# Performance work log

Measured on AMD Instinct MI355X. Metric: run time of the kernel, lower is better.

Reference implementation:

```python
import jax, jax.numpy as jnp
import numpy as np

N_SUBJECTS = 16
N_LABELS = 8
DENS_TEMP = 0.1  # args.ProtoSim_dens_temp


def setup_inputs() -> dict:
    key = jax.random.key(0)
    k1, k2, k3 = jax.random.split(key, 3)
    B, V, D = 131072, 2, 128
    X_data = jax.random.normal(k1, (B, V, D), dtype=jnp.float32)
    subject = jax.random.randint(k2, (B,), 0, N_SUBJECTS, dtype=jnp.int64) if jax.config.read('jax_enable_x64') else jax.random.randint(k2, (B,), 0, N_SUBJECTS)
    labels = jax.random.randint(k3, (B,), 0, N_LABELS)
    return {"X_data": X_data, "subject": subject, "labels": labels}


def reference(X_data, subject, labels):
    B, V, D = X_data.shape
    G = N_SUBJECTS * N_LABELS
    # torch.cat(torch.unbind(X_data, dim=1), dim=0): view-major ordering -> [V*B, D]
    cf = jnp.transpose(X_data, (1, 0, 2)).reshape(V * B, D)
    # subject/labels duplicated once (module assumes 2 views)
    seg = jnp.tile(subject * N_LABELS + labels, V)  # group id per row, [V*B]
    counts = jax.ops.segment_sum(jnp.ones((V * B,), jnp.float32), seg, num_segments=G)
    centroid = jax.ops.segment_sum(cf, seg, num_segments=G) / counts[:, None]  # [G, D]
    # per-point euclidean distance to own group centroid (torch.cdist to 1-row centroid)
    dist = jnp.linalg.norm(cf - centroid[seg], axis=1)  # [V*B]
    # density: mean(sqrt(dist)) / log(n + 10) for groups with n > 1, else 0 then dmax
    dens = (jax.ops.segment_sum(jnp.sqrt(dist), seg, num_segments=G) / counts) / jnp.log(counts + 10.0)
    dens = jnp.where(counts > 1, dens, 0.0)
    dens = jnp.where(counts > 1, dens, dens.max())
    lo = jnp.percentile(dens, 10.0)
    hi = jnp.percentile(dens, 90.0)
    dens = jnp.clip(dens, lo, hi)
    dens = DENS_TEMP * dens / dens.mean()
    cen_of_cen = centroid.mean(axis=0)  # [D]
    sim = jnp.exp((centroid @ cen_of_cen) / dens)  # [G]
    sim = sim - sim.max()
    return -sim.mean()
```

## Files before the change

kernel.cpp:

```cpp
#include <hip/hip_runtime.h>
#include <cstdint>
#include <cstddef>

#define BPTS    131072
#define D_DIM   128
#define G_GR    128
#define NL      8
#define NSLC    16
#define PERMBUF 128
#define NBLK_S  64
#define PPB     (BPTS / NBLK_S)

__global__ __launch_bounds__(256) void k_hist(const int* __restrict__ sub,
                                              const int* __restrict__ lab,
                                              int* __restrict__ hblk) {
    __shared__ int h[G_GR];
    int t = threadIdx.x, blk = blockIdx.x;
    if (t < G_GR) h[t] = 0;
    __syncthreads();
    int b0 = blk * PPB;
    for (int i = t; i < PPB; i += 256)
        atomicAdd(&h[sub[b0 + i] * NL + lab[b0 + i]], 1);
    __syncthreads();
    if (t < G_GR) hblk[blk * G_GR + t] = h[t];
}

__global__ __launch_bounds__(256) void k_scatter(const int* __restrict__ sub,
                                                 const int* __restrict__ lab,
                                                 const int* __restrict__ hblk,
                                                 int* __restrict__ counts,
                                                 int* __restrict__ offsets,
                                                 float* __restrict__ countsf,
                                                 int* __restrict__ perm) {
    __shared__ int tot[G_GR];
    __shared__ int cur[G_GR];
    int t = threadIdx.x, blk = blockIdx.x;
    if (t < G_GR) {
        int tt = 0, mine = 0;
        for (int b = 0; b < NBLK_S; ++b) {
            int v = hblk[b * G_GR + t];
            tt += v;
            if (b < blk) mine += v;
        }
        tot[t] = tt;
        cur[t] = mine;
    }
    __syncthreads();
    if (t < G_GR) {
        int off = 0;
        for (int j = 0; j < t; ++j) off += tot[j];
        cur[t] += off;
        if (blk == 0) {
            counts[t]  = tot[t];
            offsets[t] = off;
            countsf[t] = 2.0f * (float)tot[t];
        }
    }
    __syncthreads();
    int b0 = blk * PPB;
    for (int i = t; i < PPB; i += 256) {
        int p = b0 + i;
        int g = sub[p] * NL + lab[p];
        int s = atomicAdd(&cur[g], 1);
        perm[s] = p;
    }
}

__global__ __launch_bounds__(256) void k_psum(const float4* __restrict__ X4,
                                              const int* __restrict__ perm,
                                              const int* __restrict__ offsets,
                                              const int* __restrict__ counts,
                                              float* __restrict__ part) {
    __shared__ int   pbuf[PERMBUF];
    __shared__ float red[4 * 256];
    int g = blockIdx.x >> 4, s = blockIdx.x & 15;
    int off = offsets[g], len = counts[g];
    int lo = off + (len * s) / NSLC;
    int hi = off + (len * (s + 1)) / NSLC;
    int slen = hi - lo;
    int t = threadIdx.x, lane = t & 63, w = t >> 6;

    for (int j = t; j < slen; j += 256) pbuf[j] = perm[lo + j];
    __syncthreads();

    float4 acc = make_float4(0.f, 0.f, 0.f, 0.f);
    for (int i = w * 8; i < slen; i += 32) {
        int idx[8];
#pragma unroll
        for (int u = 0; u < 8; ++u) {
            int j = i + u;
            idx[u] = pbuf[(j < slen) ? j : (slen - 1)];
        }
        float4 x[8];
#pragma unroll
        for (int u = 0; u < 8; ++u) x[u] = X4[(size_t)idx[u] * 64 + lane];
#pragma unroll
        for (int u = 0; u < 8; ++u) {
            if (i + u < slen) {
                acc.x += x[u].x; acc.y += x[u].y;
                acc.z += x[u].z; acc.w += x[u].w;
            }
        }
    }
    red[w * 256 + lane * 4 + 0] = acc.x;
    red[w * 256 + lane * 4 + 1] = acc.y;
    red[w * 256 + lane * 4 + 2] = acc.z;
    red[w * 256 + lane * 4 + 3] = acc.w;
    __syncthreads();
    if (t < 128) {
        float v = 0.f;
        for (int r = 0; r < 4; ++r)
            v += red[r * 256 + t] + red[r * 256 + t + 128];
        part[(size_t)blockIdx.x * 128 + t] = v;
    }
}

__global__ __launch_bounds__(256) void k_dist(const float4* __restrict__ X4,
                                              const int* __restrict__ perm,
                                              const int* __restrict__ offsets,
                                              const int* __restrict__ counts,
                                              const float* __restrict__ part,
                                              float* __restrict__ centroid,
                                              float* __restrict__ dpart) {
    __shared__ int   pbuf[PERMBUF];
    __shared__ float cen[D_DIM];
    __shared__ float wsum[4];
    int g = blockIdx.x >> 4, s = blockIdx.x & 15;
    int off = offsets[g], len = counts[g];
    int lo = off + (len * s) / NSLC;
    int hi = off + (len * (s + 1)) / NSLC;
    int slen = hi - lo;
    int t = threadIdx.x, lane = t & 63, w = t >> 6;

    if (t < D_DIM) {
        float v = 0.f;
        for (int s2 = 0; s2 < NSLC; ++s2)
            v += part[(size_t)(g * NSLC + s2) * 128 + t];
        float c = (len > 0) ? v / (2.0f * (float)len) : 0.f;
        cen[t] = c;
        if (s == 0) centroid[g * D_DIM + t] = c;
    }
    for (int j = t; j < slen; j += 256) pbuf[j] = perm[lo + j];
    __syncthreads();

    int cd = (lane & 31) * 4;
    float4 c = make_float4(cen[cd], cen[cd + 1], cen[cd + 2], cen[cd + 3]);

    float sacc = 0.f;
    for (int i = w * 8; i < slen; i += 32) {
        int idx[8];
#pragma unroll
        for (int u = 0; u < 8; ++u) {
            int j = i + u;
            idx[u] = pbuf[(j < slen) ? j : (slen - 1)];
        }
        float4 x[8];
#pragma unroll
        for (int u = 0; u < 8; ++u) x[u] = X4[(size_t)idx[u] * 64 + lane];
#pragma unroll
        for (int u = 0; u < 8; ++u) {
            float dx = x[u].x - c.x, dy = x[u].y - c.y;
            float dz = x[u].z - c.z, dw = x[u].w - c.w;
            float d = dx * dx + dy * dy + dz * dz + dw * dw;
#pragma unroll
            for (int m = 1; m <= 16; m <<= 1) d += __shfl_xor(d, m);
            if (i + u < slen) sacc += sqrtf(sqrtf(d));
        }
    }
    float t2 = sacc + __shfl_xor(sacc, 32);
    if (lane == 0) wsum[w] = t2;
    __syncthreads();
    if (t == 0) dpart[blockIdx.x] = wsum[0] + wsum[1] + wsum[2] + wsum[3];
}

__global__ __launch_bounds__(128) void k_final(const float* __restrict__ dpart,
                                               const float* __restrict__ countsf,
                                               const float* __restrict__ centroid,
                                               float* __restrict__ out) {
    __shared__ float srt[G_GR];
    __shared__ float red[G_GR];
    __shared__ float coc[D_DIM];
    int t = threadIdx.x;

    float ds = 0.f;
    for (int s = 0; s < NSLC; ++s) ds += dpart[t * NSLC + s];
    float cnt  = countsf[t];
    float dens = (cnt > 1.f) ? (ds / cnt) / logf(cnt + 10.f) : 0.f;

    red[t] = dens;
    __syncthreads();
    for (int s = 64; s > 0; s >>= 1) {
        if (t < s) red[t] = fmaxf(red[t], red[t + s]);
        __syncthreads();
    }
    float dmax = red[0];
    __syncthreads();
    if (!(cnt > 1.f)) dens = dmax;

    srt[t] = dens;
    __syncthreads();
    for (int k = 2; k <= G_GR; k <<= 1) {
        for (int j = k >> 1; j > 0; j >>= 1) {
            int ixj = t ^ j;
            if (ixj > t) {
                float a = srt[t], b = srt[ixj];
                bool up = ((t & k) == 0);
                if ((a > b) == up) { srt[t] = b; srt[ixj] = a; }
            }
            __syncthreads();
        }
    }
    double p10 = 0.10 * 127.0, p90 = 0.90 * 127.0;
    int   i10 = (int)p10,           i90 = (int)p90;
    float f10 = (float)(p10 - i10), f90 = (float)(p90 - i90);
    float lo = srt[i10] + f10 * (srt[i10 + 1] - srt[i10]);
    float hi = srt[i90] + f90 * (srt[i90 + 1] - srt[i90]);
    dens = fminf(fmaxf(dens, lo), hi);

    red[t] = dens;
    __syncthreads();
    for (int s = 64; s > 0; s >>= 1) {
        if (t < s) red[t] += red[t + s];
        __syncthreads();
    }
    float dmean = red[0] / 128.f;
    __syncthreads();
    dens = 0.1f * dens / dmean;

    float cs = 0.f;
    for (int g = 0; g < G_GR; ++g) cs += centroid[g * D_DIM + t];
    coc[t] = cs / 128.f;
    __syncthreads();

    float dot = 0.f;
    for (int d = 0; d < D_DIM; ++d) dot += centroid[t * D_DIM + d] * coc[d];
    float sim = expf(dot / dens);

    red[t] = sim;
    __syncthreads();
    for (int s = 64; s > 0; s >>= 1) {
        if (t < s) red[t] = fmaxf(red[t], red[t + s]);
        __syncthreads();
    }
    float smax = red[0];
    __syncthreads();
    red[t] = sim - smax;
    __syncthreads();
    for (int s = 64; s > 0; s >>= 1) {
        if (t < s) red[t] += red[t + s];
        __syncthreads();
    }
    if (t == 0) out[0] = -(red[0] / 128.f);
}

extern "C" void kernel_launch(void* const* d_in, const int* in_sizes, int n_in,
                              void* d_out, int out_size, void* d_ws, size_t ws_size,
                              hipStream_t stream) {
    const float4* X4      = (const float4*)d_in[0];
    const int*    subject = (const int*)d_in[1];
    const int*    labels  = (const int*)d_in[2];
    float*        out     = (float*)d_out;
    char*         ws      = (char*)d_ws;

    size_t o = 0;
    int*   hblk     = (int*)(ws + o);   o += (size_t)NBLK_S * G_GR * 4;
    int*   counts   = (int*)(ws + o);   o += 512;
    int*   offsets  = (int*)(ws + o);   o += 512;
    float* countsf  = (float*)(ws + o); o += 512;
    int*   perm     = (int*)(ws + o);   o += (size_t)BPTS * 4;
    float* part     = (float*)(ws + o); o += (size_t)G_GR * NSLC * 128 * 4;
    float* centroid = (float*)(ws + o); o += (size_t)G_GR * D_DIM * 4;
    float* dpart    = (float*)(ws + o); o += (size_t)G_GR * NSLC * 4;

    k_hist   <<<NBLK_S, 256, 0, stream>>>(subject, labels, hblk);
    k_scatter<<<NBLK_S, 256, 0, stream>>>(subject, labels, hblk, counts, offsets, countsf, perm);
    k_psum   <<<G_GR * NSLC, 256, 0, stream>>>(X4, perm, offsets, counts, part);
    k_dist   <<<G_GR * NSLC, 256, 0, stream>>>(X4, perm, offsets, counts, part, centroid, dpart);
    k_final  <<<1, 128, 0, stream>>>(dpart, countsf, centroid, out);
}
```

Measured before the change: 240.2 us.

## Replace group sort with streaming LDS-atomic centroid and distance binning

Removes the histogram/scatter permutation and gathered per-group reads. Instead, each block streams contiguous points and accumulates per-group sums and distances into shared-memory bins with atomics. Per-block partials are then reduced by separate kernels. The trade is coalesced X reads against large partial-buffer traffic (512 copies of the 128x128 centroid bins), heavy LDS atomics, and 64KB LDS per block limiting occupancy.

Measured after the change: 300.8 us. +25.2%, slower.

```diff
diff --git a/kernel.cpp b/kernel.cpp
--- a/kernel.cpp
+++ b/kernel.cpp
@@ -6,174 +6,158 @@
 #define D_DIM   128
 #define G_GR    128
 #define NL      8
-#define NSLC    16
-#define PERMBUF 128
-#define NBLK_S  64
-#define PPB     (BPTS / NBLK_S)
-
-__global__ __launch_bounds__(256) void k_hist(const int* __restrict__ sub,
-                                              const int* __restrict__ lab,
-                                              int* __restrict__ hblk) {
-    __shared__ int h[G_GR];
+#define GD      (G_GR * D_DIM)
+#define NBLK    512
+#define TPB     512
+#define PPB     (BPTS / NBLK)
+#define PPW     (PPB / 8)
+#define DRB     16
+
+__global__ __launch_bounds__(TPB) void k_centroid(const float4* __restrict__ X4,
+                                                  const int* __restrict__ sub,
+                                                  const int* __restrict__ lab,
+                                                  float* __restrict__ cpart,
+                                                  int* __restrict__ hpart) {
+    __shared__ float bins[GD];
+    __shared__ int   hist[G_GR];
     int t = threadIdx.x, blk = blockIdx.x;
-    if (t < G_GR) h[t] = 0;
-    __syncthreads();
-    int b0 = blk * PPB;
-    for (int i = t; i < PPB; i += 256)
-        atomicAdd(&h[sub[b0 + i] * NL + lab[b0 + i]], 1);
-    __syncthreads();
-    if (t < G_GR) hblk[blk * G_GR + t] = h[t];
-}
-
-__global__ __launch_bounds__(256) void k_scatter(const int* __restrict__ sub,
-                                                 const int* __restrict__ lab,
-                                                 const int* __restrict__ hblk,
-                                                 int* __restrict__ counts,
-                                                 int* __restrict__ offsets,
-                                                 float* __restrict__ countsf,
-                                                 int* __restrict__ perm) {
-    __shared__ int tot[G_GR];
-    __shared__ int cur[G_GR];
-    int t = threadIdx.x, blk = blockIdx.x;
-    if (t < G_GR) {
-        int tt = 0, mine = 0;
-        for (int b = 0; b < NBLK_S; ++b) {
-            int v = hblk[b * G_GR + t];
-            tt += v;
-            if (b < blk) mine += v;
-        }
-        tot[t] = tt;
-        cur[t] = mine;
-    }
-    __syncthreads();
-    if (t < G_GR) {
-        int off = 0;
-        for (int j = 0; j < t; ++j) off += tot[j];
-        cur[t] += off;
-        if (blk == 0) {
-            counts[t]  = tot[t];
-            offsets[t] = off;
-            countsf[t] = 2.0f * (float)tot[t];
-        }
-    }
-    __syncthreads();
-    int b0 = blk * PPB;
-    for (int i = t; i < PPB; i += 256) {
-        int p = b0 + i;
-        int g = sub[p] * NL + lab[p];
-        int s = atomicAdd(&cur[g], 1);
-        perm[s] = p;
-    }
-}
-
-__global__ __launch_bounds__(256) void k_psum(const float4* __restrict__ X4,
-                                              const int* __restrict__ perm,
-                                              const int* __restrict__ offsets,
-                                              const int* __restrict__ counts,
-                                              float* __restrict__ part) {
-    __shared__ int   pbuf[PERMBUF];
-    __shared__ float red[4 * 256];
-    int g = blockIdx.x >> 4, s = blockIdx.x & 15;
-    int off = offsets[g], len = counts[g];
-    int lo = off + (len * s) / NSLC;
-    int hi = off + (len * (s + 1)) / NSLC;
-    int slen = hi - lo;
-    int t = threadIdx.x, lane = t & 63, w = t >> 6;
-
-    for (int j = t; j < slen; j += 256) pbuf[j] = perm[lo + j];
-    __syncthreads();
-
-    float4 acc = make_float4(0.f, 0.f, 0.f, 0.f);
-    for (int i = w * 8; i < slen; i += 32) {
-        int idx[8];
+    int lane = t & 63, w = t >> 6;
+
+    for (int i = t; i < GD; i += TPB) bins[i] = 0.f;
+    if (t < G_GR) hist[t] = 0;
+
+    int base = blk * PPB + w * PPW;
+    int pl = base + (lane & 31);
+    int gv = sub[pl] * NL + lab[pl];
+    __syncthreads();
+
+    for (int it = 0; it < PPW / 8; ++it) {
+        int p0 = base + it * 8;
+        float4 x[8];
+#pragma unroll
+        for (int u = 0; u < 8; ++u)
+            x[u] = X4[(size_t)(p0 + u) * 64 + lane];
 #pragma unroll
         for (int u = 0; u < 8; ++u) {
-            int j = i + u;
-            idx[u] = pbuf[(j < slen) ? j : (slen - 1)];
-        }
-        float4 x[8];
-#pragma unroll
-        for (int u = 0; u < 8; ++u) x[u] = X4[(size_t)idx[u] * 64 + lane];
-#pragma unroll
-        for (int u = 0; u < 8; ++u) {
-            if (i + u < slen) {
-                acc.x += x[u].x; acc.y += x[u].y;
-                acc.z += x[u].z; acc.w += x[u].w;
+            int g = __shfl(gv, it * 8 + u);
+            float4 v = x[u];
+            v.x += __shfl_xor(v.x, 32);
+            v.y += __shfl_xor(v.y, 32);
+            v.z += __shfl_xor(v.z, 32);
+            v.w += __shfl_xor(v.w, 32);
+            if (lane < 32) {
+                float* b = &bins[g * D_DIM + lane * 4];
+                atomicAdd(b + 0, v.x);
+                atomicAdd(b + 1, v.y);
+                atomicAdd(b + 2, v.z);
+                atomicAdd(b + 3, v.w);
+            } else if (lane == 32) {
+                atomicAdd(&hist[g], 1);
             }
         }
     }
-    red[w * 256 + lane * 4 + 0] = acc.x;
-    red[w * 256 + lane * 4 + 1] = acc.y;
-    red[w * 256 + lane * 4 + 2] = acc.z;
-    red[w * 256 + lane * 4 + 3] = acc.w;
-    __syncthreads();
-    if (t < 128) {
-        float v = 0.f;
-        for (int r = 0; r < 4; ++r)
-            v += red[r * 256 + t] + red[r * 256 + t + 128];
-        part[(size_t)blockIdx.x * 128 + t] = v;
-    }
-}
-
-__global__ __launch_bounds__(256) void k_dist(const float4* __restrict__ X4,
-                                              const int* __restrict__ perm,
-                                              const int* __restrict__ offsets,
-                                              const int* __restrict__ counts,
-                                              const float* __restrict__ part,
-                                              float* __restrict__ centroid,
-                                              float* __restrict__ dpart) {
-    __shared__ int   pbuf[PERMBUF];
-    __shared__ float cen[D_DIM];
-    __shared__ float wsum[4];
-    int g = blockIdx.x >> 4, s = blockIdx.x & 15;
-    int off = offsets[g], len = counts[g];
-    int lo = off + (len * s) / NSLC;
-    int hi = off + (len * (s + 1)) / NSLC;
-    int slen = hi - lo;
-    int t = threadIdx.x, lane = t & 63, w = t >> 6;
-
+    __syncthreads();
+    for (int i = t; i < GD; i += TPB)
+        cpart[(size_t)blk * GD + i] = bins[i];
+    if (t < G_GR) hpart[blk * G_GR + t] = hist[t];
+}
+
+__global__ __launch_bounds__(512) void k_reduce(const float* __restrict__ cpart,
+                                                const int* __restrict__ hpart,
+                                                float* __restrict__ centroid,
+                                                float* __restrict__ countsf) {
+    __shared__ float red[4][D_DIM];
+    __shared__ int   hred[64];
+    __shared__ float cf2s;
+    int g = blockIdx.x, t = threadIdx.x;
+    int d = t & 127, bs = t >> 7;
+
+    float acc = 0.f;
+#pragma unroll 4
+    for (int b = bs; b < NBLK; b += 4)
+        acc += cpart[(size_t)b * GD + g * D_DIM + d];
+    red[bs][d] = acc;
+
+    if (t < 64) {
+        int hacc = 0;
+        for (int b = t; b < NBLK; b += 64) hacc += hpart[b * G_GR + g];
+        hred[t] = hacc;
+    }
+    __syncthreads();
+    if (t == 0) {
+        int n = 0;
+        for (int i = 0; i < 64; ++i) n += hred[i];
+        cf2s = 2.f * (float)n;
+        countsf[g] = cf2s;
+    }
+    __syncthreads();
     if (t < D_DIM) {
-        float v = 0.f;
-        for (int s2 = 0; s2 < NSLC; ++s2)
-            v += part[(size_t)(g * NSLC + s2) * 128 + t];
-        float c = (len > 0) ? v / (2.0f * (float)len) : 0.f;
-        cen[t] = c;
-        if (s == 0) centroid[g * D_DIM + t] = c;
-    }
-    for (int j = t; j < slen; j += 256) pbuf[j] = perm[lo + j];
-    __syncthreads();
-
-    int cd = (lane & 31) * 4;
-    float4 c = make_float4(cen[cd], cen[cd + 1], cen[cd + 2], cen[cd + 3]);
-
-    float sacc = 0.f;
-    for (int i = w * 8; i < slen; i += 32) {
-        int idx[8];
+        float v = red[0][t] + red[1][t] + red[2][t] + red[3][t];
+        float cf2 = cf2s;
+        centroid[g * D_DIM + t] = (cf2 > 0.f) ? v / cf2 : 0.f;
+    }
+}
+
+__global__ __launch_bounds__(TPB) void k_distn(const float4* __restrict__ X4,
+                                               const int* __restrict__ sub,
+                                               const int* __restrict__ lab,
+                                               const float* __restrict__ centroid,
+                                               float* __restrict__ dpart) {
+    __shared__ float cen[GD];
+    __shared__ float dbin[G_GR];
+    int t = threadIdx.x, blk = blockIdx.x;
+    int lane = t & 63, w = t >> 6;
+
+    for (int i = t; i < GD; i += TPB) cen[i] = centroid[i];
+    if (t < G_GR) dbin[t] = 0.f;
+
+    int base = blk * PPB + w * PPW;
+    int pl = base + (lane & 31);
+    int gv = sub[pl] * NL + lab[pl];
+    __syncthreads();
+
+    const float4* cen4 = (const float4*)cen;
+    int ci = lane & 31;
+
+    for (int it = 0; it < PPW / 8; ++it) {
+        int p0 = base + it * 8;
+        float4 x[8];
+#pragma unroll
+        for (int u = 0; u < 8; ++u)
+            x[u] = X4[(size_t)(p0 + u) * 64 + lane];
 #pragma unroll
         for (int u = 0; u < 8; ++u) {
-            int j = i + u;
-            idx[u] = pbuf[(j < slen) ? j : (slen - 1)];
-        }
-        float4 x[8];
-#pragma unroll
-        for (int u = 0; u < 8; ++u) x[u] = X4[(size_t)idx[u] * 64 + lane];
-#pragma unroll
-        for (int u = 0; u < 8; ++u) {
+            int g = __shfl(gv, it * 8 + u);
+            float4 c = cen4[g * 32 + ci];
             float dx = x[u].x - c.x, dy = x[u].y - c.y;
             float dz = x[u].z - c.z, dw = x[u].w - c.w;
             float d = dx * dx + dy * dy + dz * dz + dw * dw;
 #pragma unroll
             for (int m = 1; m <= 16; m <<= 1) d += __shfl_xor(d, m);
-            if (i + u < slen) sacc += sqrtf(sqrtf(d));
+            float s = sqrtf(sqrtf(d));
+            s += __shfl_xor(s, 32);
+            if (lane == 0) atomicAdd(&dbin[g], s);
         }
     }
-    float t2 = sacc + __shfl_xor(sacc, 32);
-    if (lane == 0) wsum[w] = t2;
-    __syncthreads();
-    if (t == 0) dpart[blockIdx.x] = wsum[0] + wsum[1] + wsum[2] + wsum[3];
-}
-
-__global__ __launch_bounds__(128) void k_final(const float* __restrict__ dpart,
+    __syncthreads();
+    if (t < G_GR) dpart[blk * G_GR + t] = dbin[t];
+}
+
+__global__ __launch_bounds__(256) void k_dred(const float* __restrict__ dpart,
+                                              float* __restrict__ dmid) {
+    __shared__ float red[2][G_GR];
+    int t = threadIdx.x, blk = blockIdx.x;
+    int d = t & 127, h = t >> 7;
+    int b0 = blk * (NBLK / DRB);
+    float acc = 0.f;
+    for (int b = b0 + h; b < b0 + NBLK / DRB; b += 2)
+        acc += dpart[b * G_GR + d];
+    red[h][d] = acc;
+    __syncthreads();
+    if (t < G_GR) dmid[blk * G_GR + t] = red[0][t] + red[1][t];
+}
+
+__global__ __launch_bounds__(128) void k_final(const float* __restrict__ dmid,
                                                const float* __restrict__ countsf,
                                                const float* __restrict__ centroid,
                                                float* __restrict__ out) {
@@ -183,7 +167,7 @@
     int t = threadIdx.x;
 
     float ds = 0.f;
-    for (int s = 0; s < NSLC; ++s) ds += dpart[t * NSLC + s];
+    for (int b = 0; b < DRB; ++b) ds += dmid[b * G_GR + t];
     float cnt  = countsf[t];
     float dens = (cnt > 1.f) ? (ds / cnt) / logf(cnt + 10.f) : 0.f;
 
@@ -263,18 +247,16 @@
     char*         ws      = (char*)d_ws;
 
     size_t o = 0;
-    int*   hblk     = (int*)(ws + o);   o += (size_t)NBLK_S * G_GR * 4;
-    int*   counts   = (int*)(ws + o);   o += 512;
-    int*   offsets  = (int*)(ws + o);   o += 512;
+    float* cpart    = (float*)(ws + o); o += (size_t)NBLK * GD * 4;
+    int*   hpart    = (int*)(ws + o);   o += (size_t)NBLK * G_GR * 4;
+    float* centroid = (float*)(ws + o); o += (size_t)GD * 4;
     float* countsf  = (float*)(ws + o); o += 512;
-    int*   perm     = (int*)(ws + o);   o += (size_t)BPTS * 4;
-    float* part     = (float*)(ws + o); o += (size_t)G_GR * NSLC * 128 * 4;
-    float* centroid = (float*)(ws + o); o += (size_t)G_GR * D_DIM * 4;
-    float* dpart    = (float*)(ws + o); o += (size_t)G_GR * NSLC * 4;
-
-    k_hist   <<<NBLK_S, 256, 0, stream>>>(subject, labels, hblk);
-    k_scatter<<<NBLK_S, 256, 0, stream>>>(subject, labels, hblk, counts, offsets, countsf, perm);
-    k_psum   <<<G_GR * NSLC, 256, 0, stream>>>(X4, perm, offsets, counts, part);
-    k_dist   <<<G_GR * NSLC, 256, 0, stream>>>(X4, perm, offsets, counts, part, centroid, dpart);
-    k_final  <<<1, 128, 0, stream>>>(dpart, countsf, centroid, out);
-}
+    float* dpart    = (float*)(ws + o); o += (size_t)NBLK * G_GR * 4;
+    float* dmid     = (float*)(ws + o); o += (size_t)DRB * G_GR * 4;
+
+    k_centroid<<<NBLK, TPB, 0, stream>>>(X4, subject, labels, cpart, hpart);
+    k_reduce  <<<G_GR, 512, 0, stream>>>(cpart, hpart, centroid, countsf);
+    k_distn   <<<NBLK, TPB, 0, stream>>>(X4, subject, labels, centroid, dpart);
+    k_dred    <<<DRB, 256, 0, stream>>>(dpart, dmid);
+    k_final   <<<1, 128, 0, stream>>>(dmid, countsf, centroid, out);
+}
```

## Use DPP row reductions in distance kernel and parallelize final dot products

Applied to the files above, without the earlier changes.

Replaces the shuffle-xor butterfly in the per-point distance reduction with DPP row_shr/row_bcast adds, reading the per-half-wave result from lanes 31 and 63. The final kernel grows from 128 to 512 threads: the centroid column sum is split four ways, and the 128 centroid dot products are done with wave-wide DPP reductions instead of serial per-thread loops. The aim is to cut cross-lane shuffle latency in the hot loop and shorten the single-block tail. It adds DPP control-code complexity and depends on bound_ctrl and row_bcast behaving as expected on this hardware.

New measurement: 248.2 us. 1.03x slower.

```diff
diff --git a/kernel.cpp b/kernel.cpp
--- a/kernel.cpp
+++ b/kernel.cpp
@@ -10,6 +10,34 @@
 #define PERMBUF 128
 #define NBLK_S  64
 #define PPB     (BPTS / NBLK_S)
+
+__device__ __forceinline__ float dpp_add(float d, const int ctrl) {
+    int s;
+    switch (ctrl) {
+    case 0x111: s = __builtin_amdgcn_update_dpp(0, __float_as_int(d), 0x111, 0xf, 0xf, true); break;
+    case 0x112: s = __builtin_amdgcn_update_dpp(0, __float_as_int(d), 0x112, 0xf, 0xf, true); break;
+    case 0x114: s = __builtin_amdgcn_update_dpp(0, __float_as_int(d), 0x114, 0xf, 0xf, true); break;
+    case 0x118: s = __builtin_amdgcn_update_dpp(0, __float_as_int(d), 0x118, 0xf, 0xf, true); break;
+    case 0x142: s = __builtin_amdgcn_update_dpp(0, __float_as_int(d), 0x142, 0xf, 0xf, true); break;
+    default:    s = __builtin_amdgcn_update_dpp(0, __float_as_int(d), 0x143, 0xf, 0xf, true); break;
+    }
+    return d + __int_as_float(s);
+}
+
+__device__ __forceinline__ float sum32h(float d) {
+    d = dpp_add(d, 0x111);
+    d = dpp_add(d, 0x112);
+    d = dpp_add(d, 0x114);
+    d = dpp_add(d, 0x118);
+    d = dpp_add(d, 0x142);
+    return d;
+}
+
+__device__ __forceinline__ float sum64(float d) {
+    d = sum32h(d);
+    d = dpp_add(d, 0x143);
+    return d;
+}
 
 __global__ __launch_bounds__(256) void k_hist(const int* __restrict__ sub,
                                               const int* __restrict__ lab,
@@ -162,32 +190,39 @@
             float dx = x[u].x - c.x, dy = x[u].y - c.y;
             float dz = x[u].z - c.z, dw = x[u].w - c.w;
             float d = dx * dx + dy * dy + dz * dz + dw * dw;
-#pragma unroll
-            for (int m = 1; m <= 16; m <<= 1) d += __shfl_xor(d, m);
-            if (i + u < slen) sacc += sqrtf(sqrtf(d));
-        }
-    }
-    float t2 = sacc + __shfl_xor(sacc, 32);
-    if (lane == 0) wsum[w] = t2;
+            d = sum32h(d);
+            if (i + u < slen && (lane & 31) == 31)
+                sacc += sqrtf(sqrtf(d));
+        }
+    }
+    float v0 = __int_as_float(__builtin_amdgcn_readlane(__float_as_int(sacc), 31));
+    float v1 = __int_as_float(__builtin_amdgcn_readlane(__float_as_int(sacc), 63));
+    if (lane == 0) wsum[w] = v0 + v1;
     __syncthreads();
     if (t == 0) dpart[blockIdx.x] = wsum[0] + wsum[1] + wsum[2] + wsum[3];
 }
 
-__global__ __launch_bounds__(128) void k_final(const float* __restrict__ dpart,
+__global__ __launch_bounds__(512) void k_final(const float* __restrict__ dpart,
                                                const float* __restrict__ countsf,
                                                const float* __restrict__ centroid,
                                                float* __restrict__ out) {
+    __shared__ float sl4[4][G_GR];
     __shared__ float srt[G_GR];
     __shared__ float red[G_GR];
-    __shared__ float coc[D_DIM];
+    __shared__ float cocs[D_DIM];
+    __shared__ float dotv[G_GR];
     int t = threadIdx.x;
-
-    float ds = 0.f;
-    for (int s = 0; s < NSLC; ++s) ds += dpart[t * NSLC + s];
-    float cnt  = countsf[t];
-    float dens = (cnt > 1.f) ? (ds / cnt) / logf(cnt + 10.f) : 0.f;
-
-    red[t] = dens;
+    int col = t & 127, q = t >> 7;
+    int lane = t & 63, w8 = t >> 6;
+
+    float dens = 0.f, cnt = 0.f;
+    if (t < G_GR) {
+        float ds = 0.f;
+        for (int s = 0; s < NSLC; ++s) ds += dpart[t * NSLC + s];
+        cnt = countsf[t];
+        dens = (cnt > 1.f) ? (ds / cnt) / logf(cnt + 10.f) : 0.f;
+        red[t] = dens;
+    }
     __syncthreads();
     for (int s = 64; s > 0; s >>= 1) {
         if (t < s) red[t] = fmaxf(red[t], red[t + s]);
@@ -195,14 +230,14 @@
     }
     float dmax = red[0];
     __syncthreads();
-    if (!(cnt > 1.f)) dens = dmax;
-
-    srt[t] = dens;
+    if (t < G_GR && !(cnt > 1.f)) dens = dmax;
+
+    if (t < G_GR) srt[t] = dens;
     __syncthreads();
     for (int k = 2; k <= G_GR; k <<= 1) {
         for (int j = k >> 1; j > 0; j >>= 1) {
             int ixj = t ^ j;
-            if (ixj > t) {
+            if (t < G_GR && ixj > t) {
                 float a = srt[t], b = srt[ixj];
                 bool up = ((t & k) == 0);
                 if ((a > b) == up) { srt[t] = b; srt[ixj] = a; }
@@ -215,9 +250,9 @@
     float f10 = (float)(p10 - i10), f90 = (float)(p90 - i90);
     float lo = srt[i10] + f10 * (srt[i10 + 1] - srt[i10]);
     float hi = srt[i90] + f90 * (srt[i90 + 1] - srt[i90]);
-    dens = fminf(fmaxf(dens, lo), hi);
-
-    red[t] = dens;
+    if (t < G_GR) dens = fminf(fmaxf(dens, lo), hi);
+
+    if (t < G_GR) red[t] = dens;
     __syncthreads();
     for (int s = 64; s > 0; s >>= 1) {
         if (t < s) red[t] += red[t + s];
@@ -225,18 +260,33 @@
     }
     float dmean = red[0] / 128.f;
     __syncthreads();
-    dens = 0.1f * dens / dmean;
 
     float cs = 0.f;
-    for (int g = 0; g < G_GR; ++g) cs += centroid[g * D_DIM + t];
-    coc[t] = cs / 128.f;
-    __syncthreads();
-
-    float dot = 0.f;
-    for (int d = 0; d < D_DIM; ++d) dot += centroid[t * D_DIM + d] * coc[d];
-    float sim = expf(dot / dens);
-
-    red[t] = sim;
+    for (int g = q; g < G_GR; g += 4) cs += centroid[g * D_DIM + col];
+    sl4[q][col] = cs;
+    __syncthreads();
+    if (t < D_DIM)
+        cocs[t] = (sl4[0][t] + sl4[1][t] + sl4[2][t] + sl4[3][t]) / 128.f;
+    __syncthreads();
+
+    {
+        float2 co = *(const float2*)&cocs[2 * lane];
+        for (int i = 0; i < 16; ++i) {
+            int g = w8 * 16 + i;
+            float2 c = *(const float2*)(centroid + (size_t)g * D_DIM + 2 * lane);
+            float p = c.x * co.x + c.y * co.y;
+            float sm = sum64(p);
+            if (lane == 63) dotv[g] = sm;
+        }
+    }
+    __syncthreads();
+
+    float sim = 0.f;
+    if (t < G_GR) {
+        float dv = 0.1f * dens / dmean;
+        sim = expf(dotv[t] / dv);
+        red[t] = sim;
+    }
     __syncthreads();
     for (int s = 64; s > 0; s >>= 1) {
         if (t < s) red[t] = fmaxf(red[t], red[t + s]);
@@ -244,7 +294,7 @@
     }
     float smax = red[0];
     __syncthreads();
-    red[t] = sim - smax;
+    if (t < G_GR) red[t] = sim - smax;
     __syncthreads();
     for (int s = 64; s > 0; s >>= 1) {
         if (t < s) red[t] += red[t + s];
@@ -276,5 +326,5 @@
     k_scatter<<<NBLK_S, 256, 0, stream>>>(subject, labels, hblk, counts, offsets, countsf, perm);
     k_psum   <<<G_GR * NSLC, 256, 0, stream>>>(X4, perm, offsets, counts, part);
     k_dist   <<<G_GR * NSLC, 256, 0, stream>>>(X4, perm, offsets, counts, part, centroid, dpart);
-    k_final  <<<1, 128, 0, stream>>>(dpart, countsf, centroid, out);
-}
+    k_final  <<<1, 512, 0, stream>>>(dpart, countsf, centroid, out);
+}
```
